# Kernel tuning notes

Measured on AMD Instinct MI355X. Metric: run time of the kernel, lower is better.

## Reference

```python
import math
import jax, jax.numpy as jnp
import numpy as np

EMBED_DIM = 192
N_HEADS = 6
WS = 7          # window size (hardcoded by RelativeEmbedding's 13x13 table)
HW = 56         # spatial height = width (N = 56*56 = 3136)
BATCH = 32
NW = HW // WS   # windows per side = 8
WW = WS * WS    # tokens per window = 49


def _rel_indices():
    # Replicates the from-scratch Swin RelativeEmbedding index construction:
    # x = arange(1, 8, 1/7); xi = trunc(x[None]-x[:,None]); y = tile(arange(1,8), 7)
    xs = np.arange(1.0, 8.0, 1.0 / 7.0)          # 49 values
    xi = (xs[None, :] - xs[:, None]).astype(np.int32)  # trunc toward zero, in [-6, 6]
    ys = np.concatenate([np.arange(1, 8)] * 7)
    yi = (ys[None, :] - ys[:, None]).astype(np.int32)
    # torch negative indexing wraps -> emulate with mod 13
    return jnp.asarray(xi % 13), jnp.asarray(yi % 13)


def _masks():
    half = WS * (WS // 2)  # 21
    mm = np.zeros((WW, WW), dtype=np.float32)
    mm[-half:, :-half] = -np.inf
    mm[:-half, -half:] = -np.inf
    # cross_mask = rearrange(mm, '(r w1) (c w2) -> (w1 r) (w2 c)')
    cross = mm.reshape(WS, WS, WS, WS).transpose(1, 0, 3, 2).reshape(WW, WW)
    return jnp.asarray(mm), jnp.asarray(cross)


def setup_inputs() -> dict:
    key = jax.random.key(0)
    ks = jax.random.split(key, 6)
    return {
        "x": jax.random.normal(ks[0], (BATCH, HW * HW, EMBED_DIM), jnp.float32),
        "W_qkv": jax.random.normal(ks[1], (3 * EMBED_DIM, EMBED_DIM), jnp.float32) * 0.02,
        "b_qkv": jax.random.normal(ks[2], (3 * EMBED_DIM,), jnp.float32) * 0.02,
        "W_out": jax.random.normal(ks[3], (EMBED_DIM, EMBED_DIM), jnp.float32) * 0.02,
        "b_out": jax.random.normal(ks[4], (EMBED_DIM,), jnp.float32) * 0.02,
        "B_rel": jax.random.normal(ks[5], (2 * WS - 1, 2 * WS - 1), jnp.float32),
    }


def reference(x, W_qkv, b_qkv, W_out, b_out, B_rel):
    B = x.shape[0]
    hd = EMBED_DIM // N_HEADS
    xi, yi = _rel_indices()
    bias = B_rel[xi, yi]                      # (49, 49) relative position bias
    mm, cross = _masks()

    qkv = x @ W_qkv.T + b_qkv                 # (B, N, 3E)
    # 'b (h w) (c k) -> b h w c k' : channel-major, k fastest
    qkv = qkv.reshape(B, HW, HW, EMBED_DIM, 3)
    # shifted windows: source uses -window_size // 2 == -4 (asymmetric w/ reverse +3)
    qkv = jnp.roll(qkv, shift=(-(WS) // 2, -(WS) // 2), axis=(1, 2))
    # 'b (h m1) (w m2) (H E) K -> b H h w (m1 m2) E K'
    qkv = qkv.reshape(B, NW, WS, NW, WS, N_HEADS, hd, 3)
    qkv = qkv.transpose(0, 5, 1, 3, 2, 4, 6, 7).reshape(B, N_HEADS, NW, NW, WW, hd, 3)
    q, k, v = qkv[..., 0], qkv[..., 1], qkv[..., 2]

    scores = jnp.einsum('bHhwie,bHhwje->bHhwij', q, k) / math.sqrt(hd)
    scores = scores + bias                    # broadcast over (b, H, h, w)
    # shift masking: last row of windows and last column of windows
    scores = scores.at[:, :, -1, :].add(mm)
    scores = scores.at[:, :, :, -1].add(cross)

    p = jax.nn.softmax(scores, axis=-1)
    out = jnp.einsum('bHhwij,bHhwje->bHhwie', p, v)  # (B, H, nw, nw, 49, hd)
    # 'b H h w (m1 m2) E -> b (h m1) (w m2) (H E)'
    out = out.reshape(B, N_HEADS, NW, NW, WS, WS, hd)
    out = out.transpose(0, 2, 4, 3, 5, 1, 6).reshape(B, HW, HW, EMBED_DIM)
    out = jnp.roll(out, shift=(WS // 2, WS // 2), axis=(1, 2))
    out = out.reshape(B, HW * HW, EMBED_DIM)
    return out @ W_out.T + b_out
```

## Files before the change

### kernel.cpp

```cpp
#include <hip/hip_runtime.h>

typedef _Float16 f16;
typedef _Float16 f16x4 __attribute__((ext_vector_type(4)));
typedef _Float16 f16x8 __attribute__((ext_vector_type(8)));
typedef float f32x4 __attribute__((ext_vector_type(4)));

#define MFMA32(A, B, C) __builtin_amdgcn_mfma_f32_16x16x32_f16((A), (B), (C), 0, 0, 0)
#if __has_builtin(__builtin_amdgcn_mfma_f32_16x16x16_f16)
#define MFMA16(A, B, C) __builtin_amdgcn_mfma_f32_16x16x16_f16((A), (B), (C), 0, 0, 0)
#else
#define MFMA16(A, B, C) __builtin_amdgcn_mfma_f32_16x16x16f16((A), (B), (C), 0, 0, 0)
#endif

__global__ void prep_kernel(const float* __restrict__ Wq, const float* __restrict__ bqkv,
                            const float* __restrict__ Wo, const float* __restrict__ Brel,
                            f16* __restrict__ wqd, f16* __restrict__ wod,
                            float* __restrict__ bqd, f16* __restrict__ biasreg) {
  int tid = blockIdx.x * blockDim.x + threadIdx.x;
  int nthr = gridDim.x * blockDim.x;
  for (int i = tid; i < 3 * 192 * 192; i += nthr) {
    int c = i % 192, n = (i / 192) % 192, kk = i / (192 * 192);
    wqd[i] = (f16)Wq[(size_t)(n * 3 + kk) * 192 + c];
  }
  for (int i = tid; i < 192 * 192; i += nthr) wod[i] = (f16)Wo[i];
  for (int i = tid; i < 3 * 192; i += nthr) {
    int n = i % 192, kk = i / 192;
    bqd[i] = bqkv[n * 3 + kk];
  }
  for (int idx = tid; idx < 4 * 4 * 4 * 64 * 4; idx += nthr) {
    int m = idx & 3, lane = (idx >> 2) & 63, jt = (idx >> 8) & 3,
        itt = (idx >> 10) & 3, t = idx >> 12;
    int i = itt * 16 + (lane & 15);
    int j = jt * 16 + 4 * (lane >> 4) + m;
    float v = -60000.0f;
    if (i < 49 && j < 49) {
      bool msk = false;
      if (t & 2) msk |= ((i / 7 >= 4) != (j / 7 >= 4));
      if (t & 1) msk |= ((i % 7 >= 4) != (j % 7 >= 4));
      if (!msk) {
        volatile double one = 1.0;
        volatile double step = 1.0 / 7.0;
        volatile double b1 = one + step;
        volatile double delta = b1 - one;
        volatile double mj = (double)j * delta;
        volatile double sj = 1.0 + mj;
        volatile double mi = (double)i * delta;
        volatile double si = 1.0 + mi;
        double d = (double)sj - (double)si;
        int xd = (int)d;
        int yd = (j % 7) - (i % 7);
        int xm = ((xd % 13) + 13) % 13;
        int ym = ((yd % 13) + 13) % 13;
        v = Brel[xm * 13 + ym];
      }
    }
    biasreg[idx] = (f16)v;
  }
}

__launch_bounds__(768, 3)
__global__ void swin_kernel(const float* __restrict__ x,
                            const float* __restrict__ bqd,
                            const float* __restrict__ bout,
                            const f16* __restrict__ wqd,
                            const f16* __restrict__ wod,
                            const f16* __restrict__ biasreg,
                            float* __restrict__ out) {
  __shared__ __align__(16) unsigned char xsm[2 * 64 * 384];

  const int tid = threadIdx.x;
  const int bid = blockIdx.x;
  const int p  = bid >> 6;
  const int wh = (bid >> 3) & 7;
  const int ww = bid & 7;
  const int lane = tid & 63;
  const int wv = tid >> 6;
  const int t  = (wv >= 6) ? 1 : 0;
  const int hd = wv - 6 * t;
  const int lr = lane & 15;
  const int lg = lane >> 4;

#define XP(tt, row, cb) ((void*)(xsm + (tt) * 24576 + (row) * 384 + ((cb) ^ (((row) & 7) << 4))))

  {
    for (int idx = tid; idx < 2 * 49 * 48; idx += 768) {
      int tw = idx / (49 * 48), r = idx % (49 * 48);
      int tok = r / 48, c4 = r % 48;
      const float* xb = x + (size_t)(2 * p + tw) * (3136 * 192);
      int m1 = tok / 7, m2 = tok % 7;
      int y  = wh * 7 + m1 + 4; if (y  >= 56) y  -= 56;
      int xx = ww * 7 + m2 + 4; if (xx >= 56) xx -= 56;
      float4 v = *(const float4*)(xb + ((y * 56 + xx) * 192 + c4 * 4));
      f16x4 h = { (f16)v.x, (f16)v.y, (f16)v.z, (f16)v.w };
      *(f16x4*)XP(tw, tok, c4 * 8) = h;
    }
    for (int idx = tid; idx < 2 * 15 * 24; idx += 768) {
      int tw = idx / (15 * 24), r = idx % (15 * 24);
      int tok = 49 + r / 24, c8 = r % 24;
      f16x8 z = {};
      *(f16x8*)XP(tw, tok, c8 * 16) = z;
    }
  }
  __syncthreads();

  f16x4 br[4][4];
  {
    int msk = ((wh == 7) ? 2 : 0) | ((ww == 7) ? 1 : 0);
    #pragma unroll
    for (int itt = 0; itt < 4; ++itt)
      #pragma unroll
      for (int jt = 0; jt < 4; ++jt)
        br[itt][jt] = *(const f16x4*)(biasreg + ((((msk * 4 + itt) * 4 + jt) * 64 + lane) * 4));
  }

  f16x4 qtf[2][4], ktf[2][4];
  {
    f32x4 qacc[2][4], kacc[2][4];
    #pragma unroll
    for (int nt = 0; nt < 2; ++nt)
      #pragma unroll
      for (int it = 0; it < 4; ++it) {
        qacc[nt][it] = (f32x4){0.f, 0.f, 0.f, 0.f};
        kacc[nt][it] = (f32x4){0.f, 0.f, 0.f, 0.f};
      }
    #pragma unroll
    for (int ks = 0; ks < 6; ++ks) {
      f16x8 a[4];
      #pragma unroll
      for (int it = 0; it < 4; ++it)
        a[it] = *(const f16x8*)XP(t, it * 16 + lr, ks * 64 + lg * 16);
      #pragma unroll
      for (int nt = 0; nt < 2; ++nt) {
        const size_t roff = (size_t)(hd * 32 + nt * 16 + lr) * 192 + ks * 32 + lg * 8;
        f16x8 wqf = *(const f16x8*)(wqd + roff);
        f16x8 wkf = *(const f16x8*)(wqd + 192 * 192 + roff);
        #pragma unroll
        for (int it = 0; it < 4; ++it) {
          qacc[nt][it] = MFMA32(wqf, a[it], qacc[nt][it]);
          kacc[nt][it] = MFMA32(wkf, a[it], kacc[nt][it]);
        }
      }
    }
    const float SCALE = 0.17677669529663687f;
    #pragma unroll
    for (int nt = 0; nt < 2; ++nt) {
      float4 bq4 = *(const float4*)(bqd + hd * 32 + nt * 16 + 4 * lg);
      float4 bk4 = *(const float4*)(bqd + 192 + hd * 32 + nt * 16 + 4 * lg);
      #pragma unroll
      for (int it = 0; it < 4; ++it) {
        f16x4 q, k;
        q[0] = (f16)((qacc[nt][it][0] + bq4.x) * SCALE);
        q[1] = (f16)((qacc[nt][it][1] + bq4.y) * SCALE);
        q[2] = (f16)((qacc[nt][it][2] + bq4.z) * SCALE);
        q[3] = (f16)((qacc[nt][it][3] + bq4.w) * SCALE);
        k[0] = (f16)(kacc[nt][it][0] + bk4.x);
        k[1] = (f16)(kacc[nt][it][1] + bk4.y);
        k[2] = (f16)(kacc[nt][it][2] + bk4.z);
        k[3] = (f16)(kacc[nt][it][3] + bk4.w);
        qtf[nt][it] = q; ktf[nt][it] = k;
      }
    }
  }

  f32x4 sacc[4][4];
  #pragma unroll
  for (int jt = 0; jt < 4; ++jt)
    #pragma unroll
    for (int it = 0; it < 4; ++it) {
      f32x4 c = (f32x4){0.f, 0.f, 0.f, 0.f};
      c = MFMA16(ktf[0][jt], qtf[0][it], c);
      sacc[jt][it] = MFMA16(ktf[1][jt], qtf[1][it], c);
    }

  f16x4 paf[4][4];
  #pragma unroll
  for (int itt = 0; itt < 4; ++itt) {
    float sv[16];
    #pragma unroll
    for (int jt = 0; jt < 4; ++jt)
      #pragma unroll
      for (int m = 0; m < 4; ++m)
        sv[jt * 4 + m] = sacc[jt][itt][m] + (float)br[itt][jt][m];
    float mx = sv[0];
    #pragma unroll
    for (int q = 1; q < 16; ++q) mx = fmaxf(mx, sv[q]);
    mx = fmaxf(mx, __shfl_xor(mx, 16));
    mx = fmaxf(mx, __shfl_xor(mx, 32));
    float sum = 0.f;
    #pragma unroll
    for (int q = 0; q < 16; ++q) { sv[q] = __expf(sv[q] - mx); sum += sv[q]; }
    sum += __shfl_xor(sum, 16);
    sum += __shfl_xor(sum, 32);
    float rv = 1.0f / sum;
    #pragma unroll
    for (int jt = 0; jt < 4; ++jt) {
      f16x4 pk = { (f16)(sv[jt*4+0] * rv), (f16)(sv[jt*4+1] * rv),
                   (f16)(sv[jt*4+2] * rv), (f16)(sv[jt*4+3] * rv) };
      paf[jt][itt] = pk;
    }
  }

  f16x4 vf[4][2];
  {
    f32x4 vacc[4][2];
    #pragma unroll
    for (int jt = 0; jt < 4; ++jt)
      #pragma unroll
      for (int et = 0; et < 2; ++et)
        vacc[jt][et] = (f32x4){0.f, 0.f, 0.f, 0.f};
    #pragma unroll
    for (int ks = 0; ks < 6; ++ks) {
      f16x8 a[4];
      #pragma unroll
      for (int jt = 0; jt < 4; ++jt)
        a[jt] = *(const f16x8*)XP(t, jt * 16 + lr, ks * 64 + lg * 16);
      #pragma unroll
      for (int et = 0; et < 2; ++et) {
        f16x8 wvf = *(const f16x8*)(wqd + 2 * 192 * 192 +
                      (size_t)(hd * 32 + et * 16 + lr) * 192 + ks * 32 + lg * 8);
        #pragma unroll
        for (int jt = 0; jt < 4; ++jt)
          vacc[jt][et] = MFMA32(a[jt], wvf, vacc[jt][et]);
      }
    }
    #pragma unroll
    for (int et = 0; et < 2; ++et) {
      float bv = bqd[2 * 192 + hd * 32 + et * 16 + lr];
      #pragma unroll
      for (int jt = 0; jt < 4; ++jt) {
        f16x4 v;
        #pragma unroll
        for (int m = 0; m < 4; ++m) v[m] = (f16)(vacc[jt][et][m] + bv);
        vf[jt][et] = v;
      }
    }
  }

  f32x4 oacc[4][2];
  #pragma unroll
  for (int it = 0; it < 4; ++it)
    #pragma unroll
    for (int et = 0; et < 2; ++et) {
      f32x4 c = (f32x4){0.f, 0.f, 0.f, 0.f};
      #pragma unroll
      for (int jt = 0; jt < 4; ++jt)
        c = MFMA16(paf[jt][it], vf[jt][et], c);
      oacc[it][et] = c;
    }

  __syncthreads();

  #pragma unroll
  for (int it = 0; it < 4; ++it)
    #pragma unroll
    for (int et = 0; et < 2; ++et)
      #pragma unroll
      for (int m = 0; m < 4; ++m) {
        int i = it * 16 + 4 * lg + m;
        *(f16*)XP(t, i, hd * 64 + et * 32 + lr * 2) = (f16)(oacc[it][et][m]);
      }
  __syncthreads();

  f32x4 zacc[2][4];
  {
    #pragma unroll
    for (int nt = 0; nt < 2; ++nt)
      #pragma unroll
      for (int it = 0; it < 4; ++it)
        zacc[nt][it] = (f32x4){0.f, 0.f, 0.f, 0.f};
    #pragma unroll
    for (int ks = 0; ks < 6; ++ks) {
      f16x8 a[4];
      #pragma unroll
      for (int it = 0; it < 4; ++it)
        a[it] = *(const f16x8*)XP(t, it * 16 + lr, ks * 64 + lg * 16);
      #pragma unroll
      for (int nt = 0; nt < 2; ++nt) {
        f16x8 bw = *(const f16x8*)(wod + (size_t)(hd * 32 + nt * 16 + lr) * 192 + ks * 32 + lg * 8);
        #pragma unroll
        for (int it = 0; it < 4; ++it)
          zacc[nt][it] = MFMA32(a[it], bw, zacc[nt][it]);
      }
    }
  }
  __syncthreads();

  #pragma unroll
  for (int nt = 0; nt < 2; ++nt) {
    int n = hd * 32 + nt * 16 + lr;
    float bo = bout[n];
    #pragma unroll
    for (int it = 0; it < 4; ++it)
      #pragma unroll
      for (int m = 0; m < 4; ++m) {
        int i = it * 16 + 4 * lg + m;
        *(f16*)XP(t, i, n * 2) = (f16)(zacc[nt][it][m] + bo);
      }
  }
  __syncthreads();

  {
    for (int idx = tid; idx < 2 * 49 * 48; idx += 768) {
      int tw = idx / (49 * 48), r = idx % (49 * 48);
      int tok = r / 48, c4 = r % 48;
      float* outb = out + (size_t)(2 * p + tw) * (3136 * 192);
      f16x4 z = *(const f16x4*)XP(tw, tok, c4 * 8);
      int m1 = tok / 7, m2 = tok % 7;
      int y  = wh * 7 + m1 + 3; if (y  >= 56) y  -= 56;
      int xx = ww * 7 + m2 + 3; if (xx >= 56) xx -= 56;
      float4 v = { (float)z[0], (float)z[1], (float)z[2], (float)z[3] };
      *(float4*)(outb + (size_t)(y * 56 + xx) * 192 + c4 * 4) = v;
    }
  }
#undef XP
}

extern "C" void kernel_launch(void* const* d_in, const int* in_sizes, int n_in,
                              void* d_out, int out_size, void* d_ws, size_t ws_size,
                              hipStream_t stream) {
  const float* x    = (const float*)d_in[0];
  const float* Wq   = (const float*)d_in[1];
  const float* bq   = (const float*)d_in[2];
  const float* Wo   = (const float*)d_in[3];
  const float* bo   = (const float*)d_in[4];
  const float* Brel = (const float*)d_in[5];

  f16*   wqd     = (f16*)d_ws;
  f16*   wod     = (f16*)((char*)d_ws + 0x38000);
  float* bqd     = (float*)((char*)d_ws + 0x4A000);
  f16*   biasreg = (f16*)((char*)d_ws + 0x4B000);

  hipLaunchKernelGGL(prep_kernel, dim3(256), dim3(256), 0, stream,
                     Wq, bq, Wo, Brel, wqd, wod, bqd, biasreg);
  hipLaunchKernelGGL(swin_kernel, dim3(16 * 8 * 8), dim3(768), 0, stream,
                     x, bqd, bo, wqd, wod, biasreg, (float*)d_out);
}
```

Before: 155.7 us.

## Process four batch windows per block with two passes per wave

```diff
diff --git a/kernel.cpp b/kernel.cpp
--- a/kernel.cpp
+++ b/kernel.cpp
@@ -66,7 +66,7 @@
                             const f16* __restrict__ wod,
                             const f16* __restrict__ biasreg,
                             float* __restrict__ out) {
-  __shared__ __align__(16) unsigned char xsm[2 * 64 * 384];
+  __shared__ __align__(16) unsigned char xsm[4 * 64 * 384];
 
   const int tid = threadIdx.x;
   const int bid = blockIdx.x;
@@ -75,18 +75,20 @@
   const int ww = bid & 7;
   const int lane = tid & 63;
   const int wv = tid >> 6;
-  const int t  = (wv >= 6) ? 1 : 0;
-  const int hd = wv - 6 * t;
+  const int t2 = (wv >= 6) ? 1 : 0;
+  const int hd = wv - 6 * t2;
   const int lr = lane & 15;
   const int lg = lane >> 4;
+  const int W2 = 192 * 192;
 
 #define XP(tt, row, cb) ((void*)(xsm + (tt) * 24576 + (row) * 384 + ((cb) ^ (((row) & 7) << 4))))
+#define ROFF(nt, ks) ((size_t)(hd * 32 + (nt) * 16 + lr) * 192 + (ks) * 32 + lg * 8)
 
   {
-    for (int idx = tid; idx < 2 * 49 * 48; idx += 768) {
+    for (int idx = tid; idx < 4 * 49 * 48; idx += 768) {
       int tw = idx / (49 * 48), r = idx % (49 * 48);
       int tok = r / 48, c4 = r % 48;
-      const float* xb = x + (size_t)(2 * p + tw) * (3136 * 192);
+      const float* xb = x + (size_t)(4 * p + tw) * (3136 * 192);
       int m1 = tok / 7, m2 = tok % 7;
       int y  = wh * 7 + m1 + 4; if (y  >= 56) y  -= 56;
       int xx = ww * 7 + m2 + 4; if (xx >= 56) xx -= 56;
@@ -94,7 +96,7 @@
       f16x4 h = { (f16)v.x, (f16)v.y, (f16)v.z, (f16)v.w };
       *(f16x4*)XP(tw, tok, c4 * 8) = h;
     }
-    for (int idx = tid; idx < 2 * 15 * 24; idx += 768) {
+    for (int idx = tid; idx < 4 * 15 * 24; idx += 768) {
       int tw = idx / (15 * 24), r = idx % (15 * 24);
       int tok = 49 + r / 24, c8 = r % 24;
       f16x8 z = {};
@@ -113,174 +115,202 @@
         br[itt][jt] = *(const f16x4*)(biasreg + ((((msk * 4 + itt) * 4 + jt) * 64 + lane) * 4));
   }
 
-  f16x4 qtf[2][4], ktf[2][4];
+  for (int pass = 0; pass < 2; ++pass) {
+    const int tt = 2 * t2 + pass;
+
+    f16x4 qtf[2][4], ktf[2][4];
+    {
+      f32x4 qacc[2][4], kacc[2][4];
+      #pragma unroll
+      for (int nt = 0; nt < 2; ++nt)
+        #pragma unroll
+        for (int it = 0; it < 4; ++it) {
+          qacc[nt][it] = (f32x4){0.f, 0.f, 0.f, 0.f};
+          kacc[nt][it] = (f32x4){0.f, 0.f, 0.f, 0.f};
+        }
+      f16x8 cwq0 = *(const f16x8*)(wqd + ROFF(0, 0));
+      f16x8 cwq1 = *(const f16x8*)(wqd + ROFF(1, 0));
+      f16x8 cwk0 = *(const f16x8*)(wqd + W2 + ROFF(0, 0));
+      f16x8 cwk1 = *(const f16x8*)(wqd + W2 + ROFF(1, 0));
+      #pragma unroll
+      for (int ks = 0; ks < 6; ++ks) {
+        f16x8 nwq0, nwq1, nwk0, nwk1;
+        if (ks < 5) {
+          nwq0 = *(const f16x8*)(wqd + ROFF(0, ks + 1));
+          nwq1 = *(const f16x8*)(wqd + ROFF(1, ks + 1));
+          nwk0 = *(const f16x8*)(wqd + W2 + ROFF(0, ks + 1));
+          nwk1 = *(const f16x8*)(wqd + W2 + ROFF(1, ks + 1));
+        }
+        f16x8 a[4];
+        #pragma unroll
+        for (int it = 0; it < 4; ++it)
+          a[it] = *(const f16x8*)XP(tt, it * 16 + lr, ks * 64 + lg * 16);
+        #pragma unroll
+        for (int it = 0; it < 4; ++it) {
+          qacc[0][it] = MFMA32(cwq0, a[it], qacc[0][it]);
+          kacc[0][it] = MFMA32(cwk0, a[it], kacc[0][it]);
+          qacc[1][it] = MFMA32(cwq1, a[it], qacc[1][it]);
+          kacc[1][it] = MFMA32(cwk1, a[it], kacc[1][it]);
+        }
+        if (ks < 5) { cwq0 = nwq0; cwq1 = nwq1; cwk0 = nwk0; cwk1 = nwk1; }
+      }
+      const float SCALE = 0.17677669529663687f;
+      #pragma unroll
+      for (int nt = 0; nt < 2; ++nt) {
+        float4 bq4 = *(const float4*)(bqd + hd * 32 + nt * 16 + 4 * lg);
+        float4 bk4 = *(const float4*)(bqd + 192 + hd * 32 + nt * 16 + 4 * lg);
+        #pragma unroll
+        for (int it = 0; it < 4; ++it) {
+          f16x4 q, k;
+          q[0] = (f16)((qacc[nt][it][0] + bq4.x) * SCALE);
+          q[1] = (f16)((qacc[nt][it][1] + bq4.y) * SCALE);
+          q[2] = (f16)((qacc[nt][it][2] + bq4.z) * SCALE);
+          q[3] = (f16)((qacc[nt][it][3] + bq4.w) * SCALE);
+          k[0] = (f16)(kacc[nt][it][0] + bk4.x);
+          k[1] = (f16)(kacc[nt][it][1] + bk4.y);
+          k[2] = (f16)(kacc[nt][it][2] + bk4.z);
+          k[3] = (f16)(kacc[nt][it][3] + bk4.w);
+          qtf[nt][it] = q; ktf[nt][it] = k;
+        }
+      }
+    }
+
+    f32x4 sacc[4][4];
+    #pragma unroll
+    for (int jt = 0; jt < 4; ++jt)
+      #pragma unroll
+      for (int it = 0; it < 4; ++it) {
+        f32x4 c = (f32x4){0.f, 0.f, 0.f, 0.f};
+        c = MFMA16(ktf[0][jt], qtf[0][it], c);
+        sacc[jt][it] = MFMA16(ktf[1][jt], qtf[1][it], c);
+      }
+
+    f16x4 paf[4][4];
+    #pragma unroll
+    for (int itt = 0; itt < 4; ++itt) {
+      float sv[16];
+      #pragma unroll
+      for (int jt = 0; jt < 4; ++jt)
+        #pragma unroll
+        for (int m = 0; m < 4; ++m)
+          sv[jt * 4 + m] = sacc[jt][itt][m] + (float)br[itt][jt][m];
+      float mx = sv[0];
+      #pragma unroll
+      for (int q = 1; q < 16; ++q) mx = fmaxf(mx, sv[q]);
+      mx = fmaxf(mx, __shfl_xor(mx, 16));
+      mx = fmaxf(mx, __shfl_xor(mx, 32));
+      float sum = 0.f;
+      #pragma unroll
+      for (int q = 0; q < 16; ++q) { sv[q] = __expf(sv[q] - mx); sum += sv[q]; }
+      sum += __shfl_xor(sum, 16);
+      sum += __shfl_xor(sum, 32);
+      float rv = 1.0f / sum;
+      #pragma unroll
+      for (int jt = 0; jt < 4; ++jt) {
+        f16x4 pk = { (f16)(sv[jt*4+0] * rv), (f16)(sv[jt*4+1] * rv),
+                     (f16)(sv[jt*4+2] * rv), (f16)(sv[jt*4+3] * rv) };
+        paf[jt][itt] = pk;
+      }
+    }
+
+    f16x4 vf[4][2];
+    {
+      f32x4 vacc[4][2];
+      #pragma unroll
+      for (int jt = 0; jt < 4; ++jt)
+        #pragma unroll
+        for (int et = 0; et < 2; ++et)
+          vacc[jt][et] = (f32x4){0.f, 0.f, 0.f, 0.f};
+      f16x8 cwv0 = *(const f16x8*)(wqd + 2 * W2 + ROFF(0, 0));
+      f16x8 cwv1 = *(const f16x8*)(wqd + 2 * W2 + ROFF(1, 0));
+      #pragma unroll
+      for (int ks = 0; ks < 6; ++ks) {
+        f16x8 nwv0, nwv1;
+        if (ks < 5) {
+          nwv0 = *(const f16x8*)(wqd + 2 * W2 + ROFF(0, ks + 1));
+          nwv1 = *(const f16x8*)(wqd + 2 * W2 + ROFF(1, ks + 1));
+        }
+        f16x8 a[4];
+        #pragma unroll
+        for (int jt = 0; jt < 4; ++jt)
+          a[jt] = *(const f16x8*)XP(tt, jt * 16 + lr, ks * 64 + lg * 16);
+        #pragma unroll
+        for (int jt = 0; jt < 4; ++jt) {
+          vacc[jt][0] = MFMA32(a[jt], cwv0, vacc[jt][0]);
+          vacc[jt][1] = MFMA32(a[jt], cwv1, vacc[jt][1]);
+        }
+        if (ks < 5) { cwv0 = nwv0; cwv1 = nwv1; }
+      }
+      #pragma unroll
+      for (int et = 0; et < 2; ++et) {
+        float bv = bqd[2 * 192 + hd * 32 + et * 16 + lr];
+        #pragma unroll
+        for (int jt = 0; jt < 4; ++jt) {
+          f16x4 v;
+          #pragma unroll
+          for (int m = 0; m < 4; ++m) v[m] = (f16)(vacc[jt][et][m] + bv);
+          vf[jt][et] = v;
+        }
+      }
+    }
+
+    f32x4 oacc[4][2];
+    #pragma unroll
+    for (int it = 0; it < 4; ++it)
+      #pragma unroll
+      for (int et = 0; et < 2; ++et) {
+        f32x4 c = (f32x4){0.f, 0.f, 0.f, 0.f};
+        #pragma unroll
+        for (int jt = 0; jt < 4; ++jt)
+          c = MFMA16(paf[jt][it], vf[jt][et], c);
+        oacc[it][et] = c;
+      }
+
+    __syncthreads();
+
+    #pragma unroll
+    for (int it = 0; it < 4; ++it)
+      #pragma unroll
+      for (int et = 0; et < 2; ++et)
+        #pragma unroll
+        for (int m = 0; m < 4; ++m) {
+          int i = it * 16 + 4 * lg + m;
+          *(f16*)XP(tt, i, hd * 64 + et * 32 + lr * 2) = (f16)(oacc[it][et][m]);
+        }
+  }
+  __syncthreads();
+
+  f32x4 zacc[2][2][4];
   {
-    f32x4 qacc[2][4], kacc[2][4];
-    #pragma unroll
-    for (int nt = 0; nt < 2; ++nt)
-      #pragma unroll
-      for (int it = 0; it < 4; ++it) {
-        qacc[nt][it] = (f32x4){0.f, 0.f, 0.f, 0.f};
-        kacc[nt][it] = (f32x4){0.f, 0.f, 0.f, 0.f};
-      }
+    #pragma unroll
+    for (int t = 0; t < 2; ++t)
+      #pragma unroll
+      for (int nt = 0; nt < 2; ++nt)
+        #pragma unroll
+        for (int it = 0; it < 4; ++it)
+          zacc[t][nt][it] = (f32x4){0.f, 0.f, 0.f, 0.f};
+    f16x8 cbw0 = *(const f16x8*)(wod + ROFF(0, 0));
+    f16x8 cbw1 = *(const f16x8*)(wod + ROFF(1, 0));
     #pragma unroll
     for (int ks = 0; ks < 6; ++ks) {
-      f16x8 a[4];
-      #pragma unroll
-      for (int it = 0; it < 4; ++it)
-        a[it] = *(const f16x8*)XP(t, it * 16 + lr, ks * 64 + lg * 16);
-      #pragma unroll
-      for (int nt = 0; nt < 2; ++nt) {
-        const size_t roff = (size_t)(hd * 32 + nt * 16 + lr) * 192 + ks * 32 + lg * 8;
-        f16x8 wqf = *(const f16x8*)(wqd + roff);
-        f16x8 wkf = *(const f16x8*)(wqd + 192 * 192 + roff);
+      f16x8 nbw0, nbw1;
+      if (ks < 5) {
+        nbw0 = *(const f16x8*)(wod + ROFF(0, ks + 1));
+        nbw1 = *(const f16x8*)(wod + ROFF(1, ks + 1));
+      }
+      #pragma unroll
+      for (int t = 0; t < 2; ++t) {
+        f16x8 a[4];
+        #pragma unroll
+        for (int it = 0; it < 4; ++it)
+          a[it] = *(const f16x8*)XP(2 * t2 + t, it * 16 + lr, ks * 64 + lg * 16);
         #pragma unroll
         for (int it = 0; it < 4; ++it) {
-          qacc[nt][it] = MFMA32(wqf, a[it], qacc[nt][it]);
-          kacc[nt][it] = MFMA32(wkf, a[it], kacc[nt][it]);
-        }
-      }
-    }
-    const float SCALE = 0.17677669529663687f;
-    #pragma unroll
-    for (int nt = 0; nt < 2; ++nt) {
-      float4 bq4 = *(const float4*)(bqd + hd * 32 + nt * 16 + 4 * lg);
-      float4 bk4 = *(const float4*)(bqd + 192 + hd * 32 + nt * 16 + 4 * lg);
-      #pragma unroll
-      for (int it = 0; it < 4; ++it) {
-        f16x4 q, k;
-        q[0] = (f16)((qacc[nt][it][0] + bq4.x) * SCALE);
-        q[1] = (f16)((qacc[nt][it][1] + bq4.y) * SCALE);
-        q[2] = (f16)((qacc[nt][it][2] + bq4.z) * SCALE);
-        q[3] = (f16)((qacc[nt][it][3] + bq4.w) * SCALE);
-        k[0] = (f16)(kacc[nt][it][0] + bk4.x);
-        k[1] = (f16)(kacc[nt][it][1] + bk4.y);
-        k[2] = (f16)(kacc[nt][it][2] + bk4.z);
-        k[3] = (f16)(kacc[nt][it][3] + bk4.w);
-        qtf[nt][it] = q; ktf[nt][it] = k;
-      }
-    }
-  }
-
-  f32x4 sacc[4][4];
-  #pragma unroll
-  for (int jt = 0; jt < 4; ++jt)
-    #pragma unroll
-    for (int it = 0; it < 4; ++it) {
-      f32x4 c = (f32x4){0.f, 0.f, 0.f, 0.f};
-      c = MFMA16(ktf[0][jt], qtf[0][it], c);
-      sacc[jt][it] = MFMA16(ktf[1][jt], qtf[1][it], c);
-    }
-
-  f16x4 paf[4][4];
-  #pragma unroll
-  for (int itt = 0; itt < 4; ++itt) {
-    float sv[16];
-    #pragma unroll
-    for (int jt = 0; jt < 4; ++jt)
-      #pragma unroll
-      for (int m = 0; m < 4; ++m)
-        sv[jt * 4 + m] = sacc[jt][itt][m] + (float)br[itt][jt][m];
-    float mx = sv[0];
-    #pragma unroll
-    for (int q = 1; q < 16; ++q) mx = fmaxf(mx, sv[q]);
-    mx = fmaxf(mx, __shfl_xor(mx, 16));
-    mx = fmaxf(mx, __shfl_xor(mx, 32));
-    float sum = 0.f;
-    #pragma unroll
-    for (int q = 0; q < 16; ++q) { sv[q] = __expf(sv[q] - mx); sum += sv[q]; }
-    sum += __shfl_xor(sum, 16);
-    sum += __shfl_xor(sum, 32);
-    float rv = 1.0f / sum;
-    #pragma unroll
-    for (int jt = 0; jt < 4; ++jt) {
-      f16x4 pk = { (f16)(sv[jt*4+0] * rv), (f16)(sv[jt*4+1] * rv),
-                   (f16)(sv[jt*4+2] * rv), (f16)(sv[jt*4+3] * rv) };
-      paf[jt][itt] = pk;
-    }
-  }
-
-  f16x4 vf[4][2];
-  {
-    f32x4 vacc[4][2];
-    #pragma unroll
-    for (int jt = 0; jt < 4; ++jt)
-      #pragma unroll
-      for (int et = 0; et < 2; ++et)
-        vacc[jt][et] = (f32x4){0.f, 0.f, 0.f, 0.f};
-    #pragma unroll
-    for (int ks = 0; ks < 6; ++ks) {
-      f16x8 a[4];
-      #pragma unroll
-      for (int jt = 0; jt < 4; ++jt)
-        a[jt] = *(const f16x8*)XP(t, jt * 16 + lr, ks * 64 + lg * 16);
-      #pragma unroll
-      for (int et = 0; et < 2; ++et) {
-        f16x8 wvf = *(const f16x8*)(wqd + 2 * 192 * 192 +
-                      (size_t)(hd * 32 + et * 16 + lr) * 192 + ks * 32 + lg * 8);
-        #pragma unroll
-        for (int jt = 0; jt < 4; ++jt)
-          vacc[jt][et] = MFMA32(a[jt], wvf, vacc[jt][et]);
-      }
-    }
-    #pragma unroll
-    for (int et = 0; et < 2; ++et) {
-      float bv = bqd[2 * 192 + hd * 32 + et * 16 + lr];
-      #pragma unroll
-      for (int jt = 0; jt < 4; ++jt) {
-        f16x4 v;
-        #pragma unroll
-        for (int m = 0; m < 4; ++m) v[m] = (f16)(vacc[jt][et][m] + bv);
-        vf[jt][et] = v;
-      }
-    }
-  }
-
-  f32x4 oacc[4][2];
-  #pragma unroll
-  for (int it = 0; it < 4; ++it)
-    #pragma unroll
-    for (int et = 0; et < 2; ++et) {
-      f32x4 c = (f32x4){0.f, 0.f, 0.f, 0.f};
-      #pragma unroll
-      for (int jt = 0; jt < 4; ++jt)
-        c = MFMA16(paf[jt][it], vf[jt][et], c);
-      oacc[it][et] = c;
-    }
-
-  __syncthreads();
-
-  #pragma unroll
-  for (int it = 0; it < 4; ++it)
-    #pragma unroll
-    for (int et = 0; et < 2; ++et)
-      #pragma unroll
-      for (int m = 0; m < 4; ++m) {
-        int i = it * 16 + 4 * lg + m;
-        *(f16*)XP(t, i, hd * 64 + et * 32 + lr * 2) = (f16)(oacc[it][et][m]);
-      }
-  __syncthreads();
-
-  f32x4 zacc[2][4];
-  {
-    #pragma unroll
-    for (int nt = 0; nt < 2; ++nt)
-      #pragma unroll
-      for (int it = 0; it < 4; ++it)
-        zacc[nt][it] = (f32x4){0.f, 0.f, 0.f, 0.f};
-    #pragma unroll
-    for (int ks = 0; ks < 6; ++ks) {
-      f16x8 a[4];
-      #pragma unroll
-      for (int it = 0; it < 4; ++it)
-        a[it] = *(const f16x8*)XP(t, it * 16 + lr, ks * 64 + lg * 16);
-      #pragma unroll
-      for (int nt = 0; nt < 2; ++nt) {
-        f16x8 bw = *(const f16x8*)(wod + (size_t)(hd * 32 + nt * 16 + lr) * 192 + ks * 32 + lg * 8);
-        #pragma unroll
-        for (int it = 0; it < 4; ++it)
-          zacc[nt][it] = MFMA32(a[it], bw, zacc[nt][it]);
-      }
+          zacc[t][0][it] = MFMA32(a[it], cbw0, zacc[t][0][it]);
+          zacc[t][1][it] = MFMA32(a[it], cbw1, zacc[t][1][it]);
+        }
+      }
+      if (ks < 5) { cbw0 = nbw0; cbw1 = nbw1; }
     }
   }
   __syncthreads();
@@ -290,20 +320,22 @@
     int n = hd * 32 + nt * 16 + lr;
     float bo = bout[n];
     #pragma unroll
-    for (int it = 0; it < 4; ++it)
-      #pragma unroll
-      for (int m = 0; m < 4; ++m) {
-        int i = it * 16 + 4 * lg + m;
-        *(f16*)XP(t, i, n * 2) = (f16)(zacc[nt][it][m] + bo);
-      }
+    for (int t = 0; t < 2; ++t)
+      #pragma unroll
+      for (int it = 0; it < 4; ++it)
+        #pragma unroll
+        for (int m = 0; m < 4; ++m) {
+          int i = it * 16 + 4 * lg + m;
+          *(f16*)XP(2 * t2 + t, i, n * 2) = (f16)(zacc[t][nt][it][m] + bo);
+        }
   }
   __syncthreads();
 
   {
-    for (int idx = tid; idx < 2 * 49 * 48; idx += 768) {
+    for (int idx = tid; idx < 4 * 49 * 48; idx += 768) {
       int tw = idx / (49 * 48), r = idx % (49 * 48);
       int tok = r / 48, c4 = r % 48;
-      float* outb = out + (size_t)(2 * p + tw) * (3136 * 192);
+      float* outb = out + (size_t)(4 * p + tw) * (3136 * 192);
       f16x4 z = *(const f16x4*)XP(tw, tok, c4 * 8);
       int m1 = tok / 7, m2 = tok % 7;
       int y  = wh * 7 + m1 + 3; if (y  >= 56) y  -= 56;
@@ -313,6 +345,7 @@
     }
   }
 #undef XP
+#undef ROFF
 }
 
 extern "C" void kernel_launch(void* const* d_in, const int* in_sizes, int n_in,
@@ -332,6 +365,6 @@
 
   hipLaunchKernelGGL(prep_kernel, dim3(256), dim3(256), 0, stream,
                      Wq, bq, Wo, Brel, wqd, wod, bqd, biasreg);
-  hipLaunchKernelGGL(swin_kernel, dim3(16 * 8 * 8), dim3(768), 0, stream,
+  hipLaunchKernelGGL(swin_kernel, dim3(8 * 64), dim3(768), 0, stream,
                      x, bqd, bo, wqd, wod, biasreg, (float*)d_out);
 }
```

New measurement: 316.8 us. +103.5%, slower.

## Make swin kernel persistent over four window pairs with double-buffered prefetch

Applied to the files above, without the earlier changes.

```diff
diff --git a/kernel.cpp b/kernel.cpp
--- a/kernel.cpp
+++ b/kernel.cpp
@@ -66,19 +66,20 @@
                             const f16* __restrict__ wod,
                             const f16* __restrict__ biasreg,
                             float* __restrict__ out) {
-  __shared__ __align__(16) unsigned char xsm[2 * 64 * 384];
+  __shared__ __align__(16) unsigned char xsm[4 * 64 * 384];
 
   const int tid = threadIdx.x;
   const int bid = blockIdx.x;
-  const int p  = bid >> 6;
   const int wh = (bid >> 3) & 7;
   const int ww = bid & 7;
+  const int pb = (bid >> 6) * 4;
   const int lane = tid & 63;
   const int wv = tid >> 6;
-  const int t  = (wv >= 6) ? 1 : 0;
-  const int hd = wv - 6 * t;
+  const int t2 = (wv >= 6) ? 1 : 0;
+  const int hd = wv - 6 * t2;
   const int lr = lane & 15;
   const int lg = lane >> 4;
+  const int W2 = 192 * 192;
 
 #define XP(tt, row, cb) ((void*)(xsm + (tt) * 24576 + (row) * 384 + ((cb) ^ (((row) & 7) << 4))))
 
@@ -86,7 +87,7 @@
     for (int idx = tid; idx < 2 * 49 * 48; idx += 768) {
       int tw = idx / (49 * 48), r = idx % (49 * 48);
       int tok = r / 48, c4 = r % 48;
-      const float* xb = x + (size_t)(2 * p + tw) * (3136 * 192);
+      const float* xb = x + (size_t)(2 * pb + tw) * (3136 * 192);
       int m1 = tok / 7, m2 = tok % 7;
       int y  = wh * 7 + m1 + 4; if (y  >= 56) y  -= 56;
       int xx = ww * 7 + m2 + 4; if (xx >= 56) xx -= 56;
@@ -94,11 +95,14 @@
       f16x4 h = { (f16)v.x, (f16)v.y, (f16)v.z, (f16)v.w };
       *(f16x4*)XP(tw, tok, c4 * 8) = h;
     }
-    for (int idx = tid; idx < 2 * 15 * 24; idx += 768) {
-      int tw = idx / (15 * 24), r = idx % (15 * 24);
-      int tok = 49 + r / 24, c8 = r % 24;
-      f16x8 z = {};
-      *(f16x8*)XP(tw, tok, c8 * 16) = z;
+    {
+      int idx = tid;
+      if (idx < 2 * 15 * 24) {
+        int tw = idx / (15 * 24), r = idx % (15 * 24);
+        int tok = 49 + r / 24, c8 = r % 24;
+        f16x8 z = {};
+        *(f16x8*)XP(tw, tok, c8 * 16) = z;
+      }
     }
   }
   __syncthreads();
@@ -113,198 +117,242 @@
         br[itt][jt] = *(const f16x4*)(biasreg + ((((msk * 4 + itt) * 4 + jt) * 64 + lane) * 4));
   }
 
-  f16x4 qtf[2][4], ktf[2][4];
-  {
-    f32x4 qacc[2][4], kacc[2][4];
-    #pragma unroll
-    for (int nt = 0; nt < 2; ++nt)
+  for (int w = 0; w < 4; ++w) {
+    const int setb = (w & 1) * 2;
+    const int tt = setb + t2;
+
+    f16x4 qtf[2][4], ktf[2][4];
+    {
+      f32x4 qacc[2][4], kacc[2][4];
+      #pragma unroll
+      for (int nt = 0; nt < 2; ++nt)
+        #pragma unroll
+        for (int it = 0; it < 4; ++it) {
+          qacc[nt][it] = (f32x4){0.f, 0.f, 0.f, 0.f};
+          kacc[nt][it] = (f32x4){0.f, 0.f, 0.f, 0.f};
+        }
+      #pragma unroll
+      for (int ks = 0; ks < 6; ++ks) {
+        f16x8 a[4];
+        #pragma unroll
+        for (int it = 0; it < 4; ++it)
+          a[it] = *(const f16x8*)XP(tt, it * 16 + lr, ks * 64 + lg * 16);
+        #pragma unroll
+        for (int nt = 0; nt < 2; ++nt) {
+          const size_t roff = (size_t)(hd * 32 + nt * 16 + lr) * 192 + ks * 32 + lg * 8;
+          f16x8 wqf = *(const f16x8*)(wqd + roff);
+          f16x8 wkf = *(const f16x8*)(wqd + W2 + roff);
+          #pragma unroll
+          for (int it = 0; it < 4; ++it) {
+            qacc[nt][it] = MFMA32(wqf, a[it], qacc[nt][it]);
+            kacc[nt][it] = MFMA32(wkf, a[it], kacc[nt][it]);
+          }
+        }
+      }
+      const float SCALE = 0.17677669529663687f;
+      #pragma unroll
+      for (int nt = 0; nt < 2; ++nt) {
+        float4 bq4 = *(const float4*)(bqd + hd * 32 + nt * 16 + 4 * lg);
+        float4 bk4 = *(const float4*)(bqd + 192 + hd * 32 + nt * 16 + 4 * lg);
+        #pragma unroll
+        for (int it = 0; it < 4; ++it) {
+          f16x4 q, k;
+          q[0] = (f16)((qacc[nt][it][0] + bq4.x) * SCALE);
+          q[1] = (f16)((qacc[nt][it][1] + bq4.y) * SCALE);
+          q[2] = (f16)((qacc[nt][it][2] + bq4.z) * SCALE);
+          q[3] = (f16)((qacc[nt][it][3] + bq4.w) * SCALE);
+          k[0] = (f16)(kacc[nt][it][0] + bk4.x);
+          k[1] = (f16)(kacc[nt][it][1] + bk4.y);
+          k[2] = (f16)(kacc[nt][it][2] + bk4.z);
+          k[3] = (f16)(kacc[nt][it][3] + bk4.w);
+          qtf[nt][it] = q; ktf[nt][it] = k;
+        }
+      }
+    }
+
+    f32x4 sacc[4][4];
+    #pragma unroll
+    for (int jt = 0; jt < 4; ++jt)
       #pragma unroll
       for (int it = 0; it < 4; ++it) {
-        qacc[nt][it] = (f32x4){0.f, 0.f, 0.f, 0.f};
-        kacc[nt][it] = (f32x4){0.f, 0.f, 0.f, 0.f};
-      }
-    #pragma unroll
-    for (int ks = 0; ks < 6; ++ks) {
-      f16x8 a[4];
+        f32x4 c = (f32x4){0.f, 0.f, 0.f, 0.f};
+        c = MFMA16(ktf[0][jt], qtf[0][it], c);
+        sacc[jt][it] = MFMA16(ktf[1][jt], qtf[1][it], c);
+      }
+
+    f16x4 paf[4][4];
+    #pragma unroll
+    for (int itt = 0; itt < 4; ++itt) {
+      float sv[16];
+      #pragma unroll
+      for (int jt = 0; jt < 4; ++jt)
+        #pragma unroll
+        for (int m = 0; m < 4; ++m)
+          sv[jt * 4 + m] = sacc[jt][itt][m] + (float)br[itt][jt][m];
+      float mx = sv[0];
+      #pragma unroll
+      for (int q = 1; q < 16; ++q) mx = fmaxf(mx, sv[q]);
+      mx = fmaxf(mx, __shfl_xor(mx, 16));
+      mx = fmaxf(mx, __shfl_xor(mx, 32));
+      float sum = 0.f;
+      #pragma unroll
+      for (int q = 0; q < 16; ++q) { sv[q] = __expf(sv[q] - mx); sum += sv[q]; }
+      sum += __shfl_xor(sum, 16);
+      sum += __shfl_xor(sum, 32);
+      float rv = 1.0f / sum;
+      #pragma unroll
+      for (int jt = 0; jt < 4; ++jt) {
+        f16x4 pk = { (f16)(sv[jt*4+0] * rv), (f16)(sv[jt*4+1] * rv),
+                     (f16)(sv[jt*4+2] * rv), (f16)(sv[jt*4+3] * rv) };
+        paf[jt][itt] = pk;
+      }
+    }
+
+    f16x4 vf[4][2];
+    {
+      f32x4 vacc[4][2];
+      #pragma unroll
+      for (int jt = 0; jt < 4; ++jt)
+        #pragma unroll
+        for (int et = 0; et < 2; ++et)
+          vacc[jt][et] = (f32x4){0.f, 0.f, 0.f, 0.f};
+      #pragma unroll
+      for (int ks = 0; ks < 6; ++ks) {
+        f16x8 a[4];
+        #pragma unroll
+        for (int jt = 0; jt < 4; ++jt)
+          a[jt] = *(const f16x8*)XP(tt, jt * 16 + lr, ks * 64 + lg * 16);
+        #pragma unroll
+        for (int et = 0; et < 2; ++et) {
+          f16x8 wvf = *(const f16x8*)(wqd + 2 * W2 +
+                        (size_t)(hd * 32 + et * 16 + lr) * 192 + ks * 32 + lg * 8);
+          #pragma unroll
+          for (int jt = 0; jt < 4; ++jt)
+            vacc[jt][et] = MFMA32(a[jt], wvf, vacc[jt][et]);
+        }
+      }
+      #pragma unroll
+      for (int et = 0; et < 2; ++et) {
+        float bv = bqd[2 * 192 + hd * 32 + et * 16 + lr];
+        #pragma unroll
+        for (int jt = 0; jt < 4; ++jt) {
+          f16x4 v;
+          #pragma unroll
+          for (int m = 0; m < 4; ++m) v[m] = (f16)(vacc[jt][et][m] + bv);
+          vf[jt][et] = v;
+        }
+      }
+    }
+
+    f32x4 oacc[4][2];
+    #pragma unroll
+    for (int it = 0; it < 4; ++it)
+      #pragma unroll
+      for (int et = 0; et < 2; ++et) {
+        f32x4 c = (f32x4){0.f, 0.f, 0.f, 0.f};
+        #pragma unroll
+        for (int jt = 0; jt < 4; ++jt)
+          c = MFMA16(paf[jt][it], vf[jt][et], c);
+        oacc[it][et] = c;
+      }
+
+    __syncthreads();
+
+    #pragma unroll
+    for (int it = 0; it < 4; ++it)
+      #pragma unroll
+      for (int et = 0; et < 2; ++et)
+        #pragma unroll
+        for (int m = 0; m < 4; ++m) {
+          int i = it * 16 + 4 * lg + m;
+          *(f16*)XP(tt, i, hd * 64 + et * 32 + lr * 2) = (f16)(oacc[it][et][m]);
+        }
+    __syncthreads();
+
+    float4 s0, s1, s2, s3, s4, s5, s6;
+    const int nsetb = setb ^ 2;
+    if (w < 3) {
+      const float* xn = x + (size_t)(2 * (pb + w + 1)) * (3136 * 192);
+      #define STG_LOAD(K, DST)                                                   \
+        { int idx = tid + (K) * 768;                                             \
+          if ((K) < 6 || idx < 4704) {                                           \
+            int tw = idx / 2352, r = idx % 2352;                                 \
+            int tok = r / 48, c4 = r % 48;                                       \
+            int m1 = tok / 7, m2 = tok % 7;                                      \
+            int y  = wh * 7 + m1 + 4; if (y  >= 56) y  -= 56;                    \
+            int xx = ww * 7 + m2 + 4; if (xx >= 56) xx -= 56;                    \
+            DST = *(const float4*)(xn + (size_t)tw * (3136 * 192) +              \
+                                   ((y * 56 + xx) * 192 + c4 * 4));              \
+          } }
+      STG_LOAD(0, s0) STG_LOAD(1, s1) STG_LOAD(2, s2) STG_LOAD(3, s3)
+      STG_LOAD(4, s4) STG_LOAD(5, s5) STG_LOAD(6, s6)
+      #undef STG_LOAD
+    }
+
+    f32x4 zacc[2][4];
+    {
+      #pragma unroll
+      for (int nt = 0; nt < 2; ++nt)
+        #pragma unroll
+        for (int it = 0; it < 4; ++it)
+          zacc[nt][it] = (f32x4){0.f, 0.f, 0.f, 0.f};
+      #pragma unroll
+      for (int ks = 0; ks < 6; ++ks) {
+        f16x8 a[4];
+        #pragma unroll
+        for (int it = 0; it < 4; ++it)
+          a[it] = *(const f16x8*)XP(tt, it * 16 + lr, ks * 64 + lg * 16);
+        #pragma unroll
+        for (int nt = 0; nt < 2; ++nt) {
+          f16x8 bw = *(const f16x8*)(wod + (size_t)(hd * 32 + nt * 16 + lr) * 192 + ks * 32 + lg * 8);
+          #pragma unroll
+          for (int it = 0; it < 4; ++it)
+            zacc[nt][it] = MFMA32(a[it], bw, zacc[nt][it]);
+        }
+      }
+    }
+
+    if (w < 3) {
+      #define STG_WRITE(K, SRC)                                                  \
+        { int idx = tid + (K) * 768;                                             \
+          if ((K) < 6 || idx < 4704) {                                           \
+            int tw = idx / 2352, r = idx % 2352;                                 \
+            int tok = r / 48, c4 = r % 48;                                       \
+            f16x4 h = { (f16)SRC.x, (f16)SRC.y, (f16)SRC.z, (f16)SRC.w };        \
+            *(f16x4*)XP(nsetb + tw, tok, c4 * 8) = h;                            \
+          } }
+      STG_WRITE(0, s0) STG_WRITE(1, s1) STG_WRITE(2, s2) STG_WRITE(3, s3)
+      STG_WRITE(4, s4) STG_WRITE(5, s5) STG_WRITE(6, s6)
+      #undef STG_WRITE
+      int idx = tid;
+      if (idx < 2 * 15 * 24) {
+        int tw = idx / (15 * 24), r = idx % (15 * 24);
+        int tok = 49 + r / 24, c8 = r % 24;
+        f16x8 z = {};
+        *(f16x8*)XP(nsetb + tw, tok, c8 * 16) = z;
+      }
+    }
+    __syncthreads();
+
+    #pragma unroll
+    for (int nt = 0; nt < 2; ++nt) {
+      int n = hd * 32 + nt * 16 + lr;
+      float bo = bout[n];
       #pragma unroll
       for (int it = 0; it < 4; ++it)
-        a[it] = *(const f16x8*)XP(t, it * 16 + lr, ks * 64 + lg * 16);
-      #pragma unroll
-      for (int nt = 0; nt < 2; ++nt) {
-        const size_t roff = (size_t)(hd * 32 + nt * 16 + lr) * 192 + ks * 32 + lg * 8;
-        f16x8 wqf = *(const f16x8*)(wqd + roff);
-        f16x8 wkf = *(const f16x8*)(wqd + 192 * 192 + roff);
-        #pragma unroll
-        for (int it = 0; it < 4; ++it) {
-          qacc[nt][it] = MFMA32(wqf, a[it], qacc[nt][it]);
-          kacc[nt][it] = MFMA32(wkf, a[it], kacc[nt][it]);
-        }
-      }
-    }
-    const float SCALE = 0.17677669529663687f;
-    #pragma unroll
-    for (int nt = 0; nt < 2; ++nt) {
-      float4 bq4 = *(const float4*)(bqd + hd * 32 + nt * 16 + 4 * lg);
-      float4 bk4 = *(const float4*)(bqd + 192 + hd * 32 + nt * 16 + 4 * lg);
-      #pragma unroll
-      for (int it = 0; it < 4; ++it) {
-        f16x4 q, k;
-        q[0] = (f16)((qacc[nt][it][0] + bq4.x) * SCALE);
-        q[1] = (f16)((qacc[nt][it][1] + bq4.y) * SCALE);
-        q[2] = (f16)((qacc[nt][it][2] + bq4.z) * SCALE);
-        q[3] = (f16)((qacc[nt][it][3] + bq4.w) * SCALE);
-        k[0] = (f16)(kacc[nt][it][0] + bk4.x);
-        k[1] = (f16)(kacc[nt][it][1] + bk4.y);
-        k[2] = (f16)(kacc[nt][it][2] + bk4.z);
-        k[3] = (f16)(kacc[nt][it][3] + bk4.w);
-        qtf[nt][it] = q; ktf[nt][it] = k;
-      }
-    }
-  }
-
-  f32x4 sacc[4][4];
-  #pragma unroll
-  for (int jt = 0; jt < 4; ++jt)
-    #pragma unroll
-    for (int it = 0; it < 4; ++it) {
-      f32x4 c = (f32x4){0.f, 0.f, 0.f, 0.f};
-      c = MFMA16(ktf[0][jt], qtf[0][it], c);
-      sacc[jt][it] = MFMA16(ktf[1][jt], qtf[1][it], c);
-    }
-
-  f16x4 paf[4][4];
-  #pragma unroll
-  for (int itt = 0; itt < 4; ++itt) {
-    float sv[16];
-    #pragma unroll
-    for (int jt = 0; jt < 4; ++jt)
-      #pragma unroll
-      for (int m = 0; m < 4; ++m)
-        sv[jt * 4 + m] = sacc[jt][itt][m] + (float)br[itt][jt][m];
-    float mx = sv[0];
-    #pragma unroll
-    for (int q = 1; q < 16; ++q) mx = fmaxf(mx, sv[q]);
-    mx = fmaxf(mx, __shfl_xor(mx, 16));
-    mx = fmaxf(mx, __shfl_xor(mx, 32));
-    float sum = 0.f;
-    #pragma unroll
-    for (int q = 0; q < 16; ++q) { sv[q] = __expf(sv[q] - mx); sum += sv[q]; }
-    sum += __shfl_xor(sum, 16);
-    sum += __shfl_xor(sum, 32);
-    float rv = 1.0f / sum;
-    #pragma unroll
-    for (int jt = 0; jt < 4; ++jt) {
-      f16x4 pk = { (f16)(sv[jt*4+0] * rv), (f16)(sv[jt*4+1] * rv),
-                   (f16)(sv[jt*4+2] * rv), (f16)(sv[jt*4+3] * rv) };
-      paf[jt][itt] = pk;
-    }
-  }
-
-  f16x4 vf[4][2];
-  {
-    f32x4 vacc[4][2];
-    #pragma unroll
-    for (int jt = 0; jt < 4; ++jt)
-      #pragma unroll
-      for (int et = 0; et < 2; ++et)
-        vacc[jt][et] = (f32x4){0.f, 0.f, 0.f, 0.f};
-    #pragma unroll
-    for (int ks = 0; ks < 6; ++ks) {
-      f16x8 a[4];
-      #pragma unroll
-      for (int jt = 0; jt < 4; ++jt)
-        a[jt] = *(const f16x8*)XP(t, jt * 16 + lr, ks * 64 + lg * 16);
-      #pragma unroll
-      for (int et = 0; et < 2; ++et) {
-        f16x8 wvf = *(const f16x8*)(wqd + 2 * 192 * 192 +
-                      (size_t)(hd * 32 + et * 16 + lr) * 192 + ks * 32 + lg * 8);
-        #pragma unroll
-        for (int jt = 0; jt < 4; ++jt)
-          vacc[jt][et] = MFMA32(a[jt], wvf, vacc[jt][et]);
-      }
-    }
-    #pragma unroll
-    for (int et = 0; et < 2; ++et) {
-      float bv = bqd[2 * 192 + hd * 32 + et * 16 + lr];
-      #pragma unroll
-      for (int jt = 0; jt < 4; ++jt) {
-        f16x4 v;
-        #pragma unroll
-        for (int m = 0; m < 4; ++m) v[m] = (f16)(vacc[jt][et][m] + bv);
-        vf[jt][et] = v;
-      }
-    }
-  }
-
-  f32x4 oacc[4][2];
-  #pragma unroll
-  for (int it = 0; it < 4; ++it)
-    #pragma unroll
-    for (int et = 0; et < 2; ++et) {
-      f32x4 c = (f32x4){0.f, 0.f, 0.f, 0.f};
-      #pragma unroll
-      for (int jt = 0; jt < 4; ++jt)
-        c = MFMA16(paf[jt][it], vf[jt][et], c);
-      oacc[it][et] = c;
-    }
-
-  __syncthreads();
-
-  #pragma unroll
-  for (int it = 0; it < 4; ++it)
-    #pragma unroll
-    for (int et = 0; et < 2; ++et)
-      #pragma unroll
-      for (int m = 0; m < 4; ++m) {
-        int i = it * 16 + 4 * lg + m;
-        *(f16*)XP(t, i, hd * 64 + et * 32 + lr * 2) = (f16)(oacc[it][et][m]);
-      }
-  __syncthreads();
-
-  f32x4 zacc[2][4];
-  {
-    #pragma unroll
-    for (int nt = 0; nt < 2; ++nt)
-      #pragma unroll
-      for (int it = 0; it < 4; ++it)
-        zacc[nt][it] = (f32x4){0.f, 0.f, 0.f, 0.f};
-    #pragma unroll
-    for (int ks = 0; ks < 6; ++ks) {
-      f16x8 a[4];
-      #pragma unroll
-      for (int it = 0; it < 4; ++it)
-        a[it] = *(const f16x8*)XP(t, it * 16 + lr, ks * 64 + lg * 16);
-      #pragma unroll
-      for (int nt = 0; nt < 2; ++nt) {
-        f16x8 bw = *(const f16x8*)(wod + (size_t)(hd * 32 + nt * 16 + lr) * 192 + ks * 32 + lg * 8);
-        #pragma unroll
-        for (int it = 0; it < 4; ++it)
-          zacc[nt][it] = MFMA32(a[it], bw, zacc[nt][it]);
-      }
-    }
-  }
-  __syncthreads();
-
-  #pragma unroll
-  for (int nt = 0; nt < 2; ++nt) {
-    int n = hd * 32 + nt * 16 + lr;
-    float bo = bout[n];
-    #pragma unroll
-    for (int it = 0; it < 4; ++it)
-      #pragma unroll
-      for (int m = 0; m < 4; ++m) {
-        int i = it * 16 + 4 * lg + m;
-        *(f16*)XP(t, i, n * 2) = (f16)(zacc[nt][it][m] + bo);
-      }
-  }
-  __syncthreads();
-
-  {
+        #pragma unroll
+        for (int m = 0; m < 4; ++m) {
+          int i = it * 16 + 4 * lg + m;
+          *(f16*)XP(tt, i, n * 2) = (f16)(zacc[nt][it][m] + bo);
+        }
+    }
+    __syncthreads();
+
     for (int idx = tid; idx < 2 * 49 * 48; idx += 768) {
       int tw = idx / (49 * 48), r = idx % (49 * 48);
       int tok = r / 48, c4 = r % 48;
-      float* outb = out + (size_t)(2 * p + tw) * (3136 * 192);
-      f16x4 z = *(const f16x4*)XP(tw, tok, c4 * 8);
+      float* outb = out + (size_t)(2 * (pb + w) + tw) * (3136 * 192);
+      f16x4 z = *(const f16x4*)XP(setb + tw, tok, c4 * 8);
       int m1 = tok / 7, m2 = tok % 7;
       int y  = wh * 7 + m1 + 3; if (y  >= 56) y  -= 56;
       int xx = ww * 7 + m2 + 3; if (xx >= 56) xx -= 56;
@@ -332,6 +380,6 @@
 
   hipLaunchKernelGGL(prep_kernel, dim3(256), dim3(256), 0, stream,
                      Wq, bq, Wo, Brel, wqd, wod, bqd, biasreg);
-  hipLaunchKernelGGL(swin_kernel, dim3(16 * 8 * 8), dim3(768), 0, stream,
+  hipLaunchKernelGGL(swin_kernel, dim3(256), dim3(768), 0, stream,
                      x, bqd, bo, wqd, wod, biasreg, (float*)d_out);
 }
```

New measurement: 460.6 us. +195.8%, slower.
